# Kernel tuning notes

Hardware: AMD Instinct MI355X
Metric: run time of the kernel (lower is better)

## Reference

```python
import jax, jax.numpy as jnp
import numpy as np

B, C, T = 32, 64, 8192
OUT, K = 129, 32
TWO_PI = 2.0 * np.pi
DROP_THRESH = 0.1  # squared-distance threshold for channel dropping


def setup_inputs() -> dict:
    key = jax.random.key(0)
    k1, k2, k3, k4, k5 = jax.random.split(key, 5)
    X = jax.random.normal(k1, (B, C, T), dtype=jnp.float32)
    positions = jax.random.uniform(k2, (B, C, 2), dtype=jnp.float32)
    drop_idx = jax.random.randint(k3, (B,), 0, C)
    scale = 1.0 / (K * K)
    z_real = jax.random.normal(k4, (OUT, K * K), dtype=jnp.float32) * scale
    z_imag = jax.random.normal(k5, (OUT, K * K), dtype=jnp.float32) * scale
    return {"X": X, "positions": positions, "drop_idx": drop_idx,
            "z_real": z_real, "z_imag": z_imag}


def reference(X, positions, drop_idx, z_real, z_imag):
    # frequency grid: feature index f = l_idx*K + k_idx (row-major over [l, k])
    kk = jnp.arange(1, K + 1, dtype=jnp.float32)
    coef_k = jnp.tile(kk, K)            # [K*K] varies fastest
    coef_l = jnp.repeat(kk, K)          # [K*K]

    x = positions[..., 0]               # [B, C]
    y = positions[..., 1]
    # phase: [B, C, K*K]
    phase = TWO_PI * (x[..., None] * coef_k + y[..., None] * coef_l)
    cos_mat = jnp.cos(phase)
    sin_mat = jnp.sin(phase)

    # a: [B, OUT, C]
    a = (jnp.einsum('of,bcf->boc', z_real, cos_mat)
         + jnp.einsum('of,bcf->boc', z_imag, sin_mat))

    # channel drop: remove all channels within sqdist < 0.1 of the dropped electrode
    pd = positions[jnp.arange(B), drop_idx]                 # [B, 2]
    dist = jnp.sum((positions - pd[:, None, :]) ** 2, axis=-1)  # [B, C]
    keep = dist >= DROP_THRESH                              # [B, C]

    a = jnp.where(keep[:, None, :], a, -1e9)
    attn = jax.nn.softmax(a, axis=2)                        # [B, OUT, C]
    # out: [B, OUT, T]
    return jnp.einsum('boc,bct->bot', attn, X)
```

## Files before the change

### kernel.cpp

```cpp
#include <hip/hip_runtime.h>
#include <math.h>

typedef __bf16 bf16x8 __attribute__((ext_vector_type(8)));
typedef unsigned short u16x8 __attribute__((ext_vector_type(8)));
typedef float f32x4 __attribute__((ext_vector_type(4)));

namespace {
constexpr int kB   = 32;
constexpr int kC   = 64;
constexpr int kT   = 8192;
constexpr int kOUT = 129;
constexpr int kKK  = 1024;
constexpr int kNKC = 8;
constexpr int kOP  = 144;
}

__device__ inline float sin2pi(float r) {
  float o; asm("v_sin_f32 %0, %1" : "=v"(o) : "v"(r)); return o;
}
__device__ inline float cos2pi(float r) {
  float o; asm("v_cos_f32 %0, %1" : "=v"(o) : "v"(r)); return o;
}
__device__ inline unsigned short f2bf_rne(float f) {
  unsigned int u = __builtin_bit_cast(unsigned int, f);
  return (unsigned short)((u + 0x7fffu + ((u >> 16) & 1u)) >> 16);
}
__device__ inline float bf2f(unsigned short h) {
  return __builtin_bit_cast(float, (unsigned int)h << 16);
}
__device__ inline void split8(const float* v, bf16x8& hi, bf16x8& lo) {
  u16x8 h, l;
#pragma unroll
  for (int j = 0; j < 8; ++j) {
    const unsigned short hh = f2bf_rne(v[j]);
    h[j] = hh;
    l[j] = f2bf_rne(v[j] - bf2f(hh));
  }
  hi = __builtin_bit_cast(bf16x8, h);
  lo = __builtin_bit_cast(bf16x8, l);
}
__device__ inline bf16x8 ldbf8(const unsigned short* p) {
  return __builtin_bit_cast(bf16x8, *reinterpret_cast<const u16x8*>(p));
}

__global__ __launch_bounds__(256) void sa_split_z(
    const float* __restrict__ z_real, const float* __restrict__ z_imag,
    unsigned short* __restrict__ zrh, unsigned short* __restrict__ zrl,
    unsigned short* __restrict__ zih, unsigned short* __restrict__ zil)
{
  const int i = blockIdx.x * 256 + threadIdx.x;
  if (i >= 128 * kOP * 8) return;
  const int fj = i & 7;
  const int o  = (i >> 3) % kOP;
  const int fb = i / (kOP * 8);
  const int f  = fb * 8 + fj;
  float vr = 0.f, vi = 0.f;
  if (o < kOUT) {
    vr = z_real[(size_t)o * kKK + f];
    vi = z_imag[(size_t)o * kKK + f];
  }
  unsigned short h = f2bf_rne(vr);
  zrh[i] = h; zrl[i] = f2bf_rne(vr - bf2f(h));
  h = f2bf_rne(vi);
  zih[i] = h; zil[i] = f2bf_rne(vi - bf2f(h));
}

__global__ __launch_bounds__(256) void sa_cis(
    const float* __restrict__ positions,
    unsigned short* __restrict__ csh, unsigned short* __restrict__ csl,
    unsigned short* __restrict__ snh, unsigned short* __restrict__ snl)
{
  const int i = blockIdx.x * 256 + threadIdx.x;
  const int fj = i & 7;
  const int c  = (i >> 3) & 63;
  const int fb = (i >> 9) & 127;
  const int b  = i >> 16;
  const int f  = fb * 8 + fj;
  const float2 p = reinterpret_cast<const float2*>(positions)[b * kC + c];
  const float kf = (float)((f & 31) + 1);
  const float lf = (float)((f >> 5) + 1);
  const float w = __fadd_rn(__fmul_rn(p.x, kf), __fmul_rn(p.y, lf));
  const float r = w - floorf(w);
  const float cs = cos2pi(r);
  const float sn = sin2pi(r);
  unsigned short h = f2bf_rne(cs);
  csh[i] = h; csl[i] = f2bf_rne(cs - bf2f(h));
  h = f2bf_rne(sn);
  snh[i] = h; snl[i] = f2bf_rne(sn - bf2f(h));
}

__global__ __launch_bounds__(256) void sa_phase_gemm(
    const unsigned short* __restrict__ zrh, const unsigned short* __restrict__ zrl,
    const unsigned short* __restrict__ zih, const unsigned short* __restrict__ zil,
    const unsigned short* __restrict__ csh, const unsigned short* __restrict__ csl,
    const unsigned short* __restrict__ snh, const unsigned short* __restrict__ snl,
    float* __restrict__ part)
{
  const int bid = blockIdx.x;
  const int b   = bid & 31;
  const int kc  = (bid >> 5) & 7;
  const int mh  = bid >> 8;
  const int w    = threadIdx.x >> 6;
  const int lane = threadIdx.x & 63;
  const int cg   = lane >> 4;
  const int cl   = lane & 15;
  const int c    = w * 16 + cl;

  bf16x8 BcH[4], BcL[4], BsH[4], BsL[4];
#pragma unroll
  for (int ks = 0; ks < 4; ++ks) {
    const size_t off = ((size_t)(b * 128 + kc * 16 + ks * 4 + cg) * kC + c) * 8;
    BcH[ks] = ldbf8(csh + off);
    BcL[ks] = ldbf8(csl + off);
    BsH[ks] = ldbf8(snh + off);
    BsL[ks] = ldbf8(snl + off);
  }

  const int nm  = mh ? 4 : 5;
  const int ob0 = mh * 80;

#pragma unroll
  for (int m = 0; m < 5; ++m) {
    if (m < nm) {
      const int ob = ob0 + m * 16;
      const int oa = ob + cl;
      f32x4 acc = {0.f, 0.f, 0.f, 0.f};
#pragma unroll
      for (int ks = 0; ks < 4; ++ks) {
        const size_t zo = ((size_t)(kc * 16 + ks * 4 + cg) * kOP + oa) * 8;
        const bf16x8 ArH = ldbf8(zrh + zo);
        const bf16x8 ArL = ldbf8(zrl + zo);
        const bf16x8 AiH = ldbf8(zih + zo);
        const bf16x8 AiL = ldbf8(zil + zo);
        acc = __builtin_amdgcn_mfma_f32_16x16x32_bf16(ArH, BcH[ks], acc, 0, 0, 0);
        acc = __builtin_amdgcn_mfma_f32_16x16x32_bf16(ArH, BcL[ks], acc, 0, 0, 0);
        acc = __builtin_amdgcn_mfma_f32_16x16x32_bf16(ArL, BcH[ks], acc, 0, 0, 0);
        acc = __builtin_amdgcn_mfma_f32_16x16x32_bf16(AiH, BsH[ks], acc, 0, 0, 0);
        acc = __builtin_amdgcn_mfma_f32_16x16x32_bf16(AiH, BsL[ks], acc, 0, 0, 0);
        acc = __builtin_amdgcn_mfma_f32_16x16x32_bf16(AiL, BsH[ks], acc, 0, 0, 0);
      }
#pragma unroll
      for (int r = 0; r < 4; ++r) {
        const int o = ob + cg * 4 + r;
        if (o < kOUT)
          part[(((size_t)kc * kB + b) * kOUT + o) * kC + c] = acc[r];
      }
    }
  }
}

__global__ __launch_bounds__(256) void sa_softmax(
    const float* __restrict__ part,
    const float* __restrict__ positions,
    const int*   __restrict__ drop_idx,
    unsigned short* __restrict__ a_hi,
    unsigned short* __restrict__ a_lo)
{
  const int bop = blockIdx.x * 4 + (threadIdx.x >> 6);
  const int b  = bop / kOP;
  const int o  = bop - b * kOP;
  const int c  = threadIdx.x & 63;

  if (o >= kOUT) {
    a_hi[(size_t)bop * kC + c] = 0;
    a_lo[(size_t)bop * kC + c] = 0;
    return;
  }

  float a = 0.f;
#pragma unroll
  for (int fc = 0; fc < kNKC; ++fc)
    a += part[(((size_t)fc * kB + b) * kOUT + o) * kC + c];

  const float2 p  = reinterpret_cast<const float2*>(positions)[b * kC + c];
  const int    di = drop_idx[b];
  const float2 pd = reinterpret_cast<const float2*>(positions)[b * kC + di];
  const float dx = p.x - pd.x;
  const float dy = p.y - pd.y;
  const float d2 = __fadd_rn(__fmul_rn(dx, dx), __fmul_rn(dy, dy));
  if (d2 < 0.1f) a = -1e9f;

  float m = a;
#pragma unroll
  for (int off = 32; off; off >>= 1) m = fmaxf(m, __shfl_xor(m, off));
  const float e = expf(a - m);
  float s = e;
#pragma unroll
  for (int off = 32; off; off >>= 1) s += __shfl_xor(s, off);

  const float att = e / s;
  const unsigned short h = f2bf_rne(att);
  a_hi[(size_t)bop * kC + c] = h;
  a_lo[(size_t)bop * kC + c] = f2bf_rne(att - bf2f(h));
}

__global__ __launch_bounds__(256) void sa_apply_mfma(
    const float* __restrict__ X,
    const unsigned short* __restrict__ a_hi,
    const unsigned short* __restrict__ a_lo,
    float* __restrict__ out)
{
  const int b    = blockIdx.x >> 7;
  const int tc   = blockIdx.x & 127;
  const int wave = threadIdx.x >> 6;
  const int lane = threadIdx.x & 63;
  const int cl   = lane & 15;
  const int cg   = lane >> 4;
  const int t    = tc * 64 + wave * 16 + cl;

  const float* Xb = X + (size_t)b * kC * kT;
  float xv[16];
#pragma unroll
  for (int s2 = 0; s2 < 2; ++s2)
#pragma unroll
    for (int j = 0; j < 8; ++j)
      xv[s2 * 8 + j] = Xb[(size_t)(s2 * 32 + cg * 8 + j) * kT + t];

  bf16x8 Xh0, Xl0, Xh1, Xl1;
  split8(xv,     Xh0, Xl0);
  split8(xv + 8, Xh1, Xl1);

  const unsigned short* Ah = a_hi + (size_t)b * kOP * kC;
  const unsigned short* Al = a_lo + (size_t)b * kOP * kC;
  float* outb = out + (size_t)b * kOUT * kT;

#pragma unroll 3
  for (int m = 0; m < 9; ++m) {
    const int row = m * 16 + cl;
    const size_t ra = (size_t)row * kC + cg * 8;
    const bf16x8 Ah0 = ldbf8(Ah + ra);
    const bf16x8 Ah1 = ldbf8(Ah + ra + 32);
    const bf16x8 Al0 = ldbf8(Al + ra);
    const bf16x8 Al1 = ldbf8(Al + ra + 32);

    f32x4 p = {0.f, 0.f, 0.f, 0.f};
    f32x4 q = {0.f, 0.f, 0.f, 0.f};
    p = __builtin_amdgcn_mfma_f32_16x16x32_bf16(Ah0, Xh0, p, 0, 0, 0);
    q = __builtin_amdgcn_mfma_f32_16x16x32_bf16(Ah1, Xh1, q, 0, 0, 0);
    p = __builtin_amdgcn_mfma_f32_16x16x32_bf16(Al0, Xh0, p, 0, 0, 0);
    q = __builtin_amdgcn_mfma_f32_16x16x32_bf16(Al1, Xh1, q, 0, 0, 0);
    p = __builtin_amdgcn_mfma_f32_16x16x32_bf16(Ah0, Xl0, p, 0, 0, 0);
    q = __builtin_amdgcn_mfma_f32_16x16x32_bf16(Ah1, Xl1, q, 0, 0, 0);

#pragma unroll
    for (int r = 0; r < 4; ++r) {
      const int o = m * 16 + cg * 4 + r;
      if (o < kOUT)
        outb[(size_t)o * kT + t] = p[r] + q[r];
    }
  }
}

extern "C" void kernel_launch(void* const* d_in, const int* in_sizes, int n_in,
                              void* d_out, int out_size, void* d_ws, size_t ws_size,
                              hipStream_t stream) {
  (void)in_sizes; (void)n_in; (void)out_size; (void)ws_size;
  const float* X         = (const float*)d_in[0];
  const float* positions = (const float*)d_in[1];
  const int*   drop_idx  = (const int*)d_in[2];
  const float* z_real    = (const float*)d_in[3];
  const float* z_imag    = (const float*)d_in[4];
  float* out = (float*)d_out;

  char* wsb = (char*)d_ws;
  float* part = (float*)wsb;
  unsigned short* ahi = (unsigned short*)(wsb + 8454144);
  unsigned short* alo = ahi + (size_t)kB * kOP * kC;
  unsigned short* zrh = alo + (size_t)kB * kOP * kC;
  unsigned short* zrl = zrh + 147456;
  unsigned short* zih = zrl + 147456;
  unsigned short* zil = zih + 147456;
  unsigned short* csh = zil + 147456;
  unsigned short* csl = csh + 2097152;
  unsigned short* snh = csl + 2097152;
  unsigned short* snl = snh + 2097152;

  sa_split_z<<<576, 256, 0, stream>>>(z_real, z_imag, zrh, zrl, zih, zil);
  sa_cis<<<8192, 256, 0, stream>>>(positions, csh, csl, snh, snl);
  sa_phase_gemm<<<kB * kNKC * 2, 256, 0, stream>>>(zrh, zrl, zih, zil,
                                                   csh, csl, snh, snl, part);
  sa_softmax<<<kB * kOP / 4, 256, 0, stream>>>(part, positions, drop_idx, ahi, alo);
  sa_apply_mfma<<<kB * 128, 256, 0, stream>>>(X, ahi, alo, out);
}
```

Measured before the change: 278.1 us.

## Stage apply-kernel outputs in LDS for coalesced float4 stores, widen tiles

The apply kernel now processes 256 time steps per 512-thread block. Each wave handles two 16-column MFMA tiles, so every A fragment load is reused across both. Outputs are staged in shared memory in 48-row groups and then written as full-row float4 stores, replacing the scattered 4-byte per-lane stores of the MFMA output layout. The cost is about 50KB of LDS per block, two barriers per row group, and a grid four times smaller, which may reduce occupancy.

```diff
diff --git a/kernel.cpp b/kernel.cpp
--- a/kernel.cpp
+++ b/kernel.cpp
@@ -194,60 +194,82 @@
   a_lo[(size_t)bop * kC + c] = f2bf_rne(att - bf2f(h));
 }
 
-__global__ __launch_bounds__(256) void sa_apply_mfma(
+__global__ __launch_bounds__(512) void sa_apply_mfma(
     const float* __restrict__ X,
     const unsigned short* __restrict__ a_hi,
     const unsigned short* __restrict__ a_lo,
     float* __restrict__ out)
 {
-  const int b    = blockIdx.x >> 7;
-  const int tc   = blockIdx.x & 127;
+  __shared__ float s_out[48 * 260];
+
+  const int b    = blockIdx.x >> 5;
+  const int tc   = blockIdx.x & 31;
+  const int t0   = tc * 256;
   const int wave = threadIdx.x >> 6;
   const int lane = threadIdx.x & 63;
   const int cl   = lane & 15;
   const int cg   = lane >> 4;
-  const int t    = tc * 64 + wave * 16 + cl;
+  const int tw   = wave * 32;
 
   const float* Xb = X + (size_t)b * kC * kT;
-  float xv[16];
-#pragma unroll
-  for (int s2 = 0; s2 < 2; ++s2)
-#pragma unroll
-    for (int j = 0; j < 8; ++j)
-      xv[s2 * 8 + j] = Xb[(size_t)(s2 * 32 + cg * 8 + j) * kT + t];
-
-  bf16x8 Xh0, Xl0, Xh1, Xl1;
-  split8(xv,     Xh0, Xl0);
-  split8(xv + 8, Xh1, Xl1);
+  bf16x8 Xh[2][2], Xl[2][2];
+#pragma unroll
+  for (int n = 0; n < 2; ++n) {
+    const int t = t0 + tw + n * 16 + cl;
+    float xv[16];
+#pragma unroll
+    for (int s2 = 0; s2 < 2; ++s2)
+#pragma unroll
+      for (int j = 0; j < 8; ++j)
+        xv[s2 * 8 + j] = Xb[(size_t)(s2 * 32 + cg * 8 + j) * kT + t];
+    split8(xv,     Xh[n][0], Xl[n][0]);
+    split8(xv + 8, Xh[n][1], Xl[n][1]);
+  }
 
   const unsigned short* Ah = a_hi + (size_t)b * kOP * kC;
   const unsigned short* Al = a_lo + (size_t)b * kOP * kC;
   float* outb = out + (size_t)b * kOUT * kT;
 
-#pragma unroll 3
-  for (int m = 0; m < 9; ++m) {
-    const int row = m * 16 + cl;
-    const size_t ra = (size_t)row * kC + cg * 8;
-    const bf16x8 Ah0 = ldbf8(Ah + ra);
-    const bf16x8 Ah1 = ldbf8(Ah + ra + 32);
-    const bf16x8 Al0 = ldbf8(Al + ra);
-    const bf16x8 Al1 = ldbf8(Al + ra + 32);
-
-    f32x4 p = {0.f, 0.f, 0.f, 0.f};
-    f32x4 q = {0.f, 0.f, 0.f, 0.f};
-    p = __builtin_amdgcn_mfma_f32_16x16x32_bf16(Ah0, Xh0, p, 0, 0, 0);
-    q = __builtin_amdgcn_mfma_f32_16x16x32_bf16(Ah1, Xh1, q, 0, 0, 0);
-    p = __builtin_amdgcn_mfma_f32_16x16x32_bf16(Al0, Xh0, p, 0, 0, 0);
-    q = __builtin_amdgcn_mfma_f32_16x16x32_bf16(Al1, Xh1, q, 0, 0, 0);
-    p = __builtin_amdgcn_mfma_f32_16x16x32_bf16(Ah0, Xl0, p, 0, 0, 0);
-    q = __builtin_amdgcn_mfma_f32_16x16x32_bf16(Ah1, Xl1, q, 0, 0, 0);
-
-#pragma unroll
-    for (int r = 0; r < 4; ++r) {
-      const int o = m * 16 + cg * 4 + r;
-      if (o < kOUT)
-        outb[(size_t)o * kT + t] = p[r] + q[r];
+  for (int g = 0; g < 3; ++g) {
+    f32x4 acc[3][2];
+#pragma unroll
+    for (int i = 0; i < 3; ++i) {
+      const int row = (g * 3 + i) * 16 + cl;
+      const size_t ra = (size_t)row * kC + cg * 8;
+      const bf16x8 Ah0 = ldbf8(Ah + ra);
+      const bf16x8 Ah1 = ldbf8(Ah + ra + 32);
+      const bf16x8 Al0 = ldbf8(Al + ra);
+      const bf16x8 Al1 = ldbf8(Al + ra + 32);
+#pragma unroll
+      for (int n = 0; n < 2; ++n) {
+        f32x4 a4 = {0.f, 0.f, 0.f, 0.f};
+        a4 = __builtin_amdgcn_mfma_f32_16x16x32_bf16(Ah0, Xh[n][0], a4, 0, 0, 0);
+        a4 = __builtin_amdgcn_mfma_f32_16x16x32_bf16(Ah1, Xh[n][1], a4, 0, 0, 0);
+        a4 = __builtin_amdgcn_mfma_f32_16x16x32_bf16(Al0, Xh[n][0], a4, 0, 0, 0);
+        a4 = __builtin_amdgcn_mfma_f32_16x16x32_bf16(Al1, Xh[n][1], a4, 0, 0, 0);
+        a4 = __builtin_amdgcn_mfma_f32_16x16x32_bf16(Ah0, Xl[n][0], a4, 0, 0, 0);
+        a4 = __builtin_amdgcn_mfma_f32_16x16x32_bf16(Ah1, Xl[n][1], a4, 0, 0, 0);
+        acc[i][n] = a4;
+      }
     }
+
+#pragma unroll
+    for (int i = 0; i < 3; ++i)
+#pragma unroll
+      for (int n = 0; n < 2; ++n)
+#pragma unroll
+        for (int r = 0; r < 4; ++r)
+          s_out[(i * 16 + cg * 4 + r) * 260 + tw + n * 16 + cl] = acc[i][n][r];
+
+    __syncthreads();
+
+    const int nrows = (g < 2) ? 48 : 33;
+    for (int row = wave; row < nrows; row += 8) {
+      const float4 v = *reinterpret_cast<const float4*>(&s_out[row * 260 + 4 * lane]);
+      *reinterpret_cast<float4*>(&outb[(size_t)(g * 48 + row) * kT + t0 + 4 * lane]) = v;
+    }
+
+    __syncthreads();
   }
 }
 
@@ -280,5 +302,5 @@
   sa_phase_gemm<<<kB * kNKC * 2, 256, 0, stream>>>(zrh, zrl, zih, zil,
                                                    csh, csl, snh, snl, part);
   sa_softmax<<<kB * kOP / 4, 256, 0, stream>>>(part, positions, drop_idx, ahi, alo);
-  sa_apply_mfma<<<kB * 128, 256, 0, stream>>>(X, ahi, alo, out);
-}
+  sa_apply_mfma<<<kB * 32, 512, 0, stream>>>(X, ahi, alo, out);
+}
```

Result: faster. 238.2 us (-14.3%).
